# Performance work log

Measured on AMD Instinct MI355X. Metric: run time of the kernel, lower is better.

Reference implementation:

```python
import jax, jax.numpy as jnp
import numpy as np
import math

GAIN = 6.0
FREQ = 1000.0
Q = 0.707
SAMPLE_RATE = 44100


def _peaking_coeffs():
    # torchaudio.functional.equalizer_biquad coefficients (peaking EQ)
    w0 = 2.0 * math.pi * FREQ / SAMPLE_RATE
    A = math.exp(GAIN / 40.0 * math.log(10.0))
    alpha = math.sin(w0) / (2.0 * Q)
    b0 = 1.0 + alpha * A
    b1 = -2.0 * math.cos(w0)
    b2 = 1.0 - alpha * A
    a0 = 1.0 + alpha / A
    a1 = -2.0 * math.cos(w0)
    a2 = 1.0 - alpha / A
    # normalize by a0 (lfilter semantics)
    return (np.float32(b0 / a0), np.float32(b1 / a0), np.float32(b2 / a0),
            np.float32(a1 / a0), np.float32(a2 / a0))


def setup_inputs() -> dict:
    key = jax.random.key(0)
    x = jax.random.normal(key, (8, 2, 1200000), dtype=jnp.float32)
    return {"x": x}


def _biquad(x):
    # x: [B, C, T]; direct-form-I biquad with zero initial conditions
    b0, b1, b2, a1, a2 = _peaking_coeffs()
    # FIR part, fully vectorized: f[n] = b0*x[n] + b1*x[n-1] + b2*x[n-2]
    xp = jnp.pad(x, ((0, 0), (0, 0), (2, 0)))
    f = b0 * xp[..., 2:] + b1 * xp[..., 1:-1] + b2 * xp[..., :-2]
    # IIR part via scan over time: y[n] = f[n] - a1*y[n-1] - a2*y[n-2]
    f_t = jnp.moveaxis(f, -1, 0)  # [T, B, C]
    y0 = jnp.zeros(x.shape[:-1], dtype=x.dtype)

    def step(carry, ft):
        y1, y2 = carry
        y = ft - a1 * y1 - a2 * y2
        return (y, y1), y

    _, ys = jax.lax.scan(step, (y0, y0), f_t)
    return jnp.moveaxis(ys, 0, -1)  # [B, C, T]


def reference(x):
    return _biquad(x)
```

## Files before the change

kernel.cpp:

```cpp
#include <hip/hip_runtime.h>
#include <math.h>


#define T_LEN 1200000
#define NCH   16
#define L     32
#define NR    64
#define NWARM 4
#define OUT_ROWS (NR - NWARM)
#define OUT_PER_SEG (OUT_ROWS * L)
#define SEGS (T_LEN / OUT_PER_SEG)
#define WAVE_FLOATS (NR * L)
#define WPB   4
#define NBLOCKS (SEGS * NCH / WPB)

struct Params {
    float b0, b1, b2, a1, a2;
    float lnr, theta, inv_sinth;
    float C[6][4];
};

__global__ __launch_bounds__(256, 5) void eq_kernel(const float* __restrict__ x,
                                                    float* __restrict__ y, Params P)
{
    __shared__ __align__(16) float lds[WPB * WAVE_FLOATS];

    const int lane = threadIdx.x & 63;
    const int wid  = threadIdx.x >> 6;
    float* __restrict__ xs = lds + (wid << 11);

    const int wg  = blockIdx.x * WPB + wid;
    const int ch  = wg / SEGS;
    const int seg = wg - ch * SEGS;
    const float* __restrict__ xc = x + (size_t)ch * T_LEN;
    float*       __restrict__ yc = y + (size_t)ch * T_LEN;
    const int g0 = seg * OUT_PER_SEG - NWARM * L;

    float c1r[4], c2r[4];
    {
        const int t0 = (lane << 2) & 31;
        float ph[5];
        #pragma unroll
        for (int k = 0; k < 5; ++k) {
            int t = t0 - 1 + k;
            ph[k] = (t < 0) ? 0.f
                            : expf(t * P.lnr) * sinf((t + 1) * P.theta) * P.inv_sinth;
        }
        #pragma unroll
        for (int k = 0; k < 4; ++k) {
            c1r[k] = fmaf(-P.a1, ph[k + 1], -P.a2 * ph[k]);
            c2r[k] = -P.a2 * ph[k + 1];
        }
    }

    #pragma unroll
    for (int it = 0; it < WAVE_FLOATS / 4 / 64; ++it) {
        int q = ((it << 6) + lane) << 2;
        int g = g0 + q;
        float4 val = make_float4(0.f, 0.f, 0.f, 0.f);
        if (g >= 0 && g < T_LEN) val = *(const float4*)(xc + g);
        int row = q >> 5, j = q & 31, m = row & 31, base = row << 5;
        xs[base + ((j + 0) ^ m)] = val.x;
        xs[base + ((j + 1) ^ m)] = val.y;
        xs[base + ((j + 2) ^ m)] = val.z;
        xs[base + ((j + 3) ^ m)] = val.w;
    }
    asm volatile("" ::: "memory");

    float v1 = 0.f, v2 = 0.f;
    {
        const int m = lane & 31, base = lane << 5;
        float x1 = 0.f, x2 = 0.f;
        if (lane > 0) {
            int pb = (lane - 1) << 5, pm = (lane - 1) & 31;
            x1 = xs[pb + (31 ^ pm)];
            x2 = xs[pb + (30 ^ pm)];
        }
        asm volatile("" ::: "memory");
        #pragma unroll 8
        for (int j = 0; j < L; ++j) {
            int w = base + (j ^ m);
            float xv = xs[w];
            float f  = fmaf(P.b0, xv, fmaf(P.b1, x1, P.b2 * x2));
            float t2 = fmaf(-P.a2, v2, f);
            float yv = fmaf(-P.a1, v1, t2);
            v2 = v1; v1 = yv;
            x2 = x1; x1 = xv;
            xs[w] = yv;
        }
    }

    #pragma unroll
    for (int k = 0; k < 6; ++k) {
        int d = 1 << k;
        float p1 = __shfl_up(v1, d);
        float p2 = __shfl_up(v2, d);
        if (lane < d) { p1 = 0.f; p2 = 0.f; }
        float n1 = fmaf(P.C[k][0], p1, fmaf(P.C[k][1], p2, v1));
        float n2 = fmaf(P.C[k][2], p1, fmaf(P.C[k][3], p2, v2));
        v1 = n1; v2 = n2;
    }
    float e1 = __shfl_up(v1, 1);
    float e2 = __shfl_up(v2, 1);
    if (lane == 0) { e1 = 0.f; e2 = 0.f; }
    asm volatile("" ::: "memory");

    const int j = (lane << 2) & 31;
    #pragma unroll
    for (int it = 0; it < 8; ++it) {
        int vo = (it << 6) + lane;
        int row = 4 + (it << 3) + (lane >> 3);
        row = row > 63 ? 63 : row;
        float al = __shfl(e1, row);
        float be = __shfl(e2, row);
        if (vo < OUT_PER_SEG / 4) {
            int m = row & 31, base = row << 5;
            float4 o;
            o.x = fmaf(al, c1r[0], fmaf(be, c2r[0], xs[base + ((j + 0) ^ m)]));
            o.y = fmaf(al, c1r[1], fmaf(be, c2r[1], xs[base + ((j + 1) ^ m)]));
            o.z = fmaf(al, c1r[2], fmaf(be, c2r[2], xs[base + ((j + 2) ^ m)]));
            o.w = fmaf(al, c1r[3], fmaf(be, c2r[3], xs[base + ((j + 3) ^ m)]));
            int q = (vo << 2) + NWARM * L;
            *(float4*)(yc + g0 + q) = o;
        }
    }
}

extern "C" void kernel_launch(void* const* d_in, const int* in_sizes, int n_in,
                              void* d_out, int out_size, void* d_ws, size_t ws_size,
                              hipStream_t stream) {
    const float* x = (const float*)d_in[0];
    float* y = (float*)d_out;

    double w0    = 2.0 * M_PI * 1000.0 / 44100.0;
    double A     = exp(6.0 / 40.0 * log(10.0));
    double al    = sin(w0) / (2.0 * 0.707);
    double b0 = 1.0 + al * A;
    double b1 = -2.0 * cos(w0);
    double b2 = 1.0 - al * A;
    double a0 = 1.0 + al / A;
    double a1 = -2.0 * cos(w0);
    double a2 = 1.0 - al / A;
    b0 /= a0; b1 /= a0; b2 /= a0; a1 /= a0; a2 /= a0;

    Params P;
    P.b0 = (float)b0; P.b1 = (float)b1; P.b2 = (float)b2;
    P.a1 = (float)a1; P.a2 = (float)a2;

    double r     = sqrt(a2);
    double theta = acos(-a1 / (2.0 * r));
    P.lnr = (float)log(r);
    P.theta = (float)theta;
    P.inv_sinth = (float)(1.0 / sin(theta));

    double m00 = -a1, m01 = -a2, m10 = 1.0, m11 = 0.0;
    for (int s = 0; s < 5; ++s) {
        double t00 = m00 * m00 + m01 * m10;
        double t01 = m00 * m01 + m01 * m11;
        double t10 = m10 * m00 + m11 * m10;
        double t11 = m10 * m01 + m11 * m11;
        m00 = t00; m01 = t01; m10 = t10; m11 = t11;
    }
    for (int k = 0; k < 6; ++k) {
        P.C[k][0] = (float)m00; P.C[k][1] = (float)m01;
        P.C[k][2] = (float)m10; P.C[k][3] = (float)m11;
        double t00 = m00 * m00 + m01 * m10;
        double t01 = m00 * m01 + m01 * m11;
        double t10 = m10 * m00 + m11 * m10;
        double t11 = m10 * m01 + m11 * m11;
        m00 = t00; m01 = t01; m10 = t10; m11 = t11;
    }

    eq_kernel<<<NBLOCKS, 256, 0, stream>>>(x, y, P);
}
```

Before: 35.36 us.

## Process two segments per wave with prefetch, padded LDS rows and vector LDS access

Each wave now handles two segments, loading the second segment's input into registers up front so its global loads overlap the first segment's scan. The XOR-swizzled LDS layout is replaced by rows padded to 36 floats, which allows float4 LDS reads and writes in the sequential scan. Output stores use nontemporal hints, and launch bounds drop to 4 blocks per CU. The cost is higher register pressure from holding 16 float4 prefetch registers, half as many blocks, and possible LDS bank conflicts from the padded stride.

Result: faster. 29.53 us (-16.5%).

```diff
diff --git a/kernel.cpp b/kernel.cpp
--- a/kernel.cpp
+++ b/kernel.cpp
@@ -1,6 +1,8 @@
 #include <hip/hip_runtime.h>
 #include <math.h>
 
+
+typedef float f32x4 __attribute__((ext_vector_type(4)));
 
 #define T_LEN 1200000
 #define NCH   16
@@ -10,9 +12,11 @@
 #define OUT_ROWS (NR - NWARM)
 #define OUT_PER_SEG (OUT_ROWS * L)
 #define SEGS (T_LEN / OUT_PER_SEG)
-#define WAVE_FLOATS (NR * L)
-#define WPB   4
-#define NBLOCKS (SEGS * NCH / WPB)
+#define WPB 4
+#define NBLOCKS 1250
+#define NWAVES (NBLOCKS * WPB)
+#define RSTRIDE 36
+#define WAVE_LDS (NR * RSTRIDE)
 
 struct Params {
     float b0, b1, b2, a1, a2;
@@ -20,21 +24,103 @@
     float C[6][4];
 };
 
-__global__ __launch_bounds__(256, 5) void eq_kernel(const float* __restrict__ x,
+__device__ __forceinline__ void load_seg(f32x4 r[8], const float* __restrict__ xc,
+                                         int g0, int lane)
+{
+    #pragma unroll
+    for (int it = 0; it < 8; ++it) {
+        int g = g0 + (it << 8) + (lane << 2);
+        f32x4 v = {0.f, 0.f, 0.f, 0.f};
+        if (g >= 0 && g < T_LEN) v = *(const f32x4*)(xc + g);
+        r[it] = v;
+    }
+}
+
+__device__ __forceinline__ void stage_seg(float* __restrict__ xs, const f32x4 r[8],
+                                          int lane)
+{
+    const int row0 = lane >> 3, j = (lane & 7) << 2;
+    #pragma unroll
+    for (int it = 0; it < 8; ++it) {
+        int row = (it << 3) + row0;
+        *(f32x4*)&xs[row * RSTRIDE + j] = r[it];
+    }
+}
+
+__device__ __forceinline__ void process_seg(float* __restrict__ xs,
+                                            float* __restrict__ yc, int g0, int lane,
+                                            const Params& P,
+                                            const float c1r[4], const float c2r[4])
+{
+    const int base = lane * RSTRIDE;
+
+    float x1 = 0.f, x2 = 0.f;
+    if (lane > 0) {
+        x1 = xs[base - RSTRIDE + 31];
+        x2 = xs[base - RSTRIDE + 30];
+    }
+    asm volatile("" ::: "memory");
+
+    float v1 = 0.f, v2 = 0.f;
+    #pragma unroll
+    for (int b = 0; b < 8; ++b) {
+        f32x4 xv = *(const f32x4*)&xs[base + (b << 2)];
+        f32x4 yv;
+        #pragma unroll
+        for (int k = 0; k < 4; ++k) {
+            float xk = xv[k];
+            float f  = fmaf(P.b0, xk, fmaf(P.b1, x1, P.b2 * x2));
+            float t2 = fmaf(-P.a2, v2, f);
+            float yk = fmaf(-P.a1, v1, t2);
+            v2 = v1; v1 = yk;
+            x2 = x1; x1 = xk;
+            yv[k] = yk;
+        }
+        *(f32x4*)&xs[base + (b << 2)] = yv;
+    }
+
+    #pragma unroll
+    for (int k = 0; k < 6; ++k) {
+        int d = 1 << k;
+        float p1 = __shfl_up(v1, d);
+        float p2 = __shfl_up(v2, d);
+        if (lane < d) { p1 = 0.f; p2 = 0.f; }
+        float n1 = fmaf(P.C[k][0], p1, fmaf(P.C[k][1], p2, v1));
+        float n2 = fmaf(P.C[k][2], p1, fmaf(P.C[k][3], p2, v2));
+        v1 = n1; v2 = n2;
+    }
+    float e1 = __shfl_up(v1, 1);
+    float e2 = __shfl_up(v2, 1);
+    if (lane == 0) { e1 = 0.f; e2 = 0.f; }
+
+    const int j0 = (lane << 2) & 31;
+    #pragma unroll
+    for (int it = 0; it < 8; ++it) {
+        int vo = (it << 6) + lane;
+        int row = NWARM + (it << 3) + (lane >> 3);
+        row = row > 63 ? 63 : row;
+        float al = __shfl(e1, row);
+        float be = __shfl(e2, row);
+        if (vo < OUT_PER_SEG / 4) {
+            f32x4 yv = *(const f32x4*)&xs[row * RSTRIDE + j0];
+            f32x4 o;
+            #pragma unroll
+            for (int k = 0; k < 4; ++k)
+                o[k] = fmaf(al, c1r[k], fmaf(be, c2r[k], yv[k]));
+            int q = (vo << 2) + NWARM * L;
+            __builtin_nontemporal_store(o, (f32x4*)(yc + g0 + q));
+        }
+    }
+}
+
+__global__ __launch_bounds__(256, 4) void eq_kernel(const float* __restrict__ x,
                                                     float* __restrict__ y, Params P)
 {
-    __shared__ __align__(16) float lds[WPB * WAVE_FLOATS];
-
+    __shared__ __align__(16) float lds[WPB * WAVE_LDS];
     const int lane = threadIdx.x & 63;
     const int wid  = threadIdx.x >> 6;
-    float* __restrict__ xs = lds + (wid << 11);
-
-    const int wg  = blockIdx.x * WPB + wid;
-    const int ch  = wg / SEGS;
-    const int seg = wg - ch * SEGS;
-    const float* __restrict__ xc = x + (size_t)ch * T_LEN;
-    float*       __restrict__ yc = y + (size_t)ch * T_LEN;
-    const int g0 = seg * OUT_PER_SEG - NWARM * L;
+    float* xs = lds + wid * WAVE_LDS;
+    const int w = blockIdx.x * WPB + wid;
 
     float c1r[4], c2r[4];
     {
@@ -53,77 +139,25 @@
         }
     }
 
-    #pragma unroll
-    for (int it = 0; it < WAVE_FLOATS / 4 / 64; ++it) {
-        int q = ((it << 6) + lane) << 2;
-        int g = g0 + q;
-        float4 val = make_float4(0.f, 0.f, 0.f, 0.f);
-        if (g >= 0 && g < T_LEN) val = *(const float4*)(xc + g);
-        int row = q >> 5, j = q & 31, m = row & 31, base = row << 5;
-        xs[base + ((j + 0) ^ m)] = val.x;
-        xs[base + ((j + 1) ^ m)] = val.y;
-        xs[base + ((j + 2) ^ m)] = val.z;
-        xs[base + ((j + 3) ^ m)] = val.w;
-    }
+    const int sA = w, sB = w + NWAVES;
+    const int chA = sA / SEGS, segA = sA - chA * SEGS;
+    const int chB = sB / SEGS, segB = sB - chB * SEGS;
+    const int g0A = segA * OUT_PER_SEG - NWARM * L;
+    const int g0B = segB * OUT_PER_SEG - NWARM * L;
+    const float* xcA = x + (size_t)chA * T_LEN;
+    const float* xcB = x + (size_t)chB * T_LEN;
+    float* ycA = y + (size_t)chA * T_LEN;
+    float* ycB = y + (size_t)chB * T_LEN;
+
+    f32x4 ra[8], rb[8];
+    load_seg(ra, xcA, g0A, lane);
+    load_seg(rb, xcB, g0B, lane);
+    stage_seg(xs, ra, lane);
     asm volatile("" ::: "memory");
-
-    float v1 = 0.f, v2 = 0.f;
-    {
-        const int m = lane & 31, base = lane << 5;
-        float x1 = 0.f, x2 = 0.f;
-        if (lane > 0) {
-            int pb = (lane - 1) << 5, pm = (lane - 1) & 31;
-            x1 = xs[pb + (31 ^ pm)];
-            x2 = xs[pb + (30 ^ pm)];
-        }
-        asm volatile("" ::: "memory");
-        #pragma unroll 8
-        for (int j = 0; j < L; ++j) {
-            int w = base + (j ^ m);
-            float xv = xs[w];
-            float f  = fmaf(P.b0, xv, fmaf(P.b1, x1, P.b2 * x2));
-            float t2 = fmaf(-P.a2, v2, f);
-            float yv = fmaf(-P.a1, v1, t2);
-            v2 = v1; v1 = yv;
-            x2 = x1; x1 = xv;
-            xs[w] = yv;
-        }
-    }
-
-    #pragma unroll
-    for (int k = 0; k < 6; ++k) {
-        int d = 1 << k;
-        float p1 = __shfl_up(v1, d);
-        float p2 = __shfl_up(v2, d);
-        if (lane < d) { p1 = 0.f; p2 = 0.f; }
-        float n1 = fmaf(P.C[k][0], p1, fmaf(P.C[k][1], p2, v1));
-        float n2 = fmaf(P.C[k][2], p1, fmaf(P.C[k][3], p2, v2));
-        v1 = n1; v2 = n2;
-    }
-    float e1 = __shfl_up(v1, 1);
-    float e2 = __shfl_up(v2, 1);
-    if (lane == 0) { e1 = 0.f; e2 = 0.f; }
+    process_seg(xs, ycA, g0A, lane, P, c1r, c2r);
+    stage_seg(xs, rb, lane);
     asm volatile("" ::: "memory");
-
-    const int j = (lane << 2) & 31;
-    #pragma unroll
-    for (int it = 0; it < 8; ++it) {
-        int vo = (it << 6) + lane;
-        int row = 4 + (it << 3) + (lane >> 3);
-        row = row > 63 ? 63 : row;
-        float al = __shfl(e1, row);
-        float be = __shfl(e2, row);
-        if (vo < OUT_PER_SEG / 4) {
-            int m = row & 31, base = row << 5;
-            float4 o;
-            o.x = fmaf(al, c1r[0], fmaf(be, c2r[0], xs[base + ((j + 0) ^ m)]));
-            o.y = fmaf(al, c1r[1], fmaf(be, c2r[1], xs[base + ((j + 1) ^ m)]));
-            o.z = fmaf(al, c1r[2], fmaf(be, c2r[2], xs[base + ((j + 2) ^ m)]));
-            o.w = fmaf(al, c1r[3], fmaf(be, c2r[3], xs[base + ((j + 3) ^ m)]));
-            int q = (vo << 2) + NWARM * L;
-            *(float4*)(yc + g0 + q) = o;
-        }
-    }
+    process_seg(xs, ycB, g0B, lane, P, c1r, c2r);
 }
 
 extern "C" void kernel_launch(void* const* d_in, const int* in_sizes, int n_in,
```
